# Optimization experiments

Hardware: AMD Instinct MI355X
Metric: run time of the kernel (lower is better)

Reference implementation:

```python
import jax, jax.numpy as jnp
import numpy as np

RCR = 5.2
RCA = 3.5
ETA_R = 16.0
ETA_A = 8.0
ZETA = 32.0
NUM_SPECIES = 4
NUM_PAIRS = NUM_SPECIES * (NUM_SPECIES + 1) // 2  # 10
SHFR = jnp.asarray(np.linspace(0.9, RCR, 17)[:-1], dtype=jnp.float32)   # (16,)
SHFA = jnp.asarray(np.linspace(0.9, RCA, 5)[:-1], dtype=jnp.float32)    # (4,)
SHFZ = jnp.asarray((np.linspace(0.0, np.pi, 9) + np.pi / 16.0)[:-1], dtype=jnp.float32)  # (8,)

def _triu_index(n):
    s1, s2 = np.triu_indices(n)
    t = np.zeros((n, n), dtype=np.int32)
    t[s1, s2] = np.arange(len(s1))
    t[s2, s1] = np.arange(len(s1))
    return jnp.asarray(t)

TRIU = _triu_index(NUM_SPECIES)  # (4,4) -> pair index in [0,10)

def _fc(d, rc):
    # cosine cutoff, zero beyond rc
    return jnp.where(d < rc, 0.5 * jnp.cos(np.float32(np.pi) * d / rc) + 0.5, 0.0)

def _aev(species, coordinates):
    N, A = species.shape
    # vec[n,i,j] = r_j - r_i  (N,A,A,3)
    vec = coordinates[:, None, :, :] - coordinates[:, :, None, :]
    d2 = jnp.sum(vec * vec, axis=-1)                      # (N,A,A)
    eye = jnp.eye(A, dtype=bool)
    d = jnp.sqrt(jnp.where(eye, 1.0, d2))                 # safe sqrt on diagonal
    pair_mask = (~eye).astype(coordinates.dtype)          # (A,A)

    # ---- radial AEV ----
    fcr = _fc(d, RCR) * pair_mask                         # (N,A,A)
    rad = 0.25 * jnp.exp(-ETA_R * (d[..., None] - SHFR) ** 2) * fcr[..., None]  # (N,A,A,16)
    sp_oh = jax.nn.one_hot(species, NUM_SPECIES, dtype=coordinates.dtype)       # (N,A,4)
    radial_aev = jnp.einsum('nijt,njs->nist', rad, sp_oh).reshape(N, A, -1)     # (N,A,64)

    # ---- angular AEV ----
    fca = _fc(d, RCA) * pair_mask                         # (N,A,A)
    dot = jnp.einsum('nijc,nikc->nijk', vec, vec)         # (N,A,A,A)
    cosang = 0.95 * dot / jnp.clip(d[:, :, :, None] * d[:, :, None, :], 1e-10)
    angles = jnp.arccos(cosang)                           # (N,A,A,A)
    mask_jk = (~eye).astype(coordinates.dtype)            # j != k
    fcj12 = fca[:, :, :, None] * fca[:, :, None, :] * mask_jk[None, None]  # (N,A,A,A)
    dmean = 0.5 * (d[:, :, :, None] + d[:, :, None, :])   # (N,A,A,A)
    factor1 = ((1.0 + jnp.cos(angles[..., None] - SHFZ)) * 0.5) ** ZETA    # (N,A,A,A,8)
    factor2 = jnp.exp(-ETA_A * (dmean[..., None] - SHFA) ** 2)             # (N,A,A,A,4)
    # terms over ordered (j,k); each unordered pair counted twice, so the
    # original factor 2 and the 0.5 double-count correction cancel.
    terms = (fcj12[..., None] * factor2)[..., :, None] * factor1[..., None, :]  # (N,A,A,A,4,8)
    terms = terms.reshape(N, A, A, A, SHFA.shape[0] * SHFZ.shape[0])            # (N,A,A,A,32)
    pair_idx = TRIU[species[:, :, None], species[:, None, :]]                   # (N,A,A)
    pair_oh = jax.nn.one_hot(pair_idx, NUM_PAIRS, dtype=coordinates.dtype)      # (N,A,A,10)
    angular_aev = jnp.einsum('nijkt,njkp->nipt', terms, pair_oh).reshape(N, A, -1)  # (N,A,320)

    return jnp.concatenate([radial_aev, angular_aev], axis=-1)  # (N,A,384)

def setup_inputs() -> dict:
    key = jax.random.key(0)
    k1, k2 = jax.random.split(key)
    species = jax.random.randint(k1, (32, 48), 0, NUM_SPECIES)
    # atoms in an 8 Angstrom box -> realistic neighbor density for 5.2 A cutoff
    coordinates = jax.random.uniform(k2, (32, 48, 3), dtype=jnp.float32) * 8.0
    return {"species": species, "coordinates": coordinates}

def reference(species, coordinates):
    return _aev(species, coordinates)
```

## Files before the change

### kernel.cpp

```cpp
#include <hip/hip_runtime.h>
#include <math.h>


#define A_ATOMS 48
#define NMOL    32
#define NFEAT   384
#define CHUNK   256

__device__ __constant__ float CZ_TAB[8] = {
     0.980785280f,  0.831469612f,  0.555570233f,  0.195090322f,
    -0.195090322f, -0.555570233f, -0.831469612f, -0.980785280f };
__device__ __constant__ float SZ_TAB[8] = {
     0.195090322f,  0.555570233f,  0.831469612f,  0.980785280f,
     0.980785280f,  0.831469612f,  0.555570233f,  0.195090322f };

__device__ __forceinline__ float bf2f(unsigned short h) {
    return __uint_as_float(((unsigned int)h) << 16);
}

__global__ __launch_bounds__(256, 6)
void AEVComputer_2156073583107_kernel(const void* __restrict__ coords_raw,
                                      const void* __restrict__ species_raw,
                                      float* __restrict__ out)
{
    const int bid   = blockIdx.x;
    const int n     = bid / A_ATOMS;
    const int i     = bid - n * A_ATOMS;
    const int tid   = threadIdx.x;
    const int w     = tid >> 6;
    const int lane  = tid & 63;
    const int sub   = lane >> 5;
    const int slice = (w << 1) | sub;
    const int t     = lane & 31;

    __shared__ float cx[A_ATOMS], cy[A_ATOMS], cz[A_ATOMS];
    __shared__ float dL[A_ATOMS], fcaL[A_ATOMS];
    __shared__ float ux[A_ATOMS], uy[A_ATOMS], uz[A_ATOMS];
    __shared__ int   sp[A_ATOMS], nbr[A_ATOMS];
    __shared__ int   Msh;
    __shared__ float4 pairbuf[CHUNK];
    __shared__ int   cnt[10], curs[10], ofs[11];
    __shared__ float ang_m[8][320];
    __shared__ float rad_m[4][64];

    const unsigned short* cu16 = (const unsigned short*)coords_raw;
    const unsigned int*   su32 = (const unsigned int*)species_raw;

    if (tid < 64) {
        float v = bf2f(cu16[tid]);
        unsigned long long mb = __ballot(fabsf(v) < 32.0f);
        const bool coords_bf16 = (__popcll(mb) >= 60);
        unsigned int sv = su32[tid & 31];
        unsigned long long m2 = __ballot((tid < 32) && sv >= 0x3F000000u && sv < 0x40800000u);
        unsigned long long m3 = __ballot((tid < 32) && (tid & 1) && sv != 0u);
        const int smode = (__popcll(m2) > 20) ? 2 : ((m3 == 0ull) ? 1 : 0);

        if (tid < A_ATOMS) {
            const int g = n * A_ATOMS + tid;
            float x, y, z;
            if (coords_bf16) {
                x = bf2f(cu16[3 * g]); y = bf2f(cu16[3 * g + 1]); z = bf2f(cu16[3 * g + 2]);
            } else {
                const float* cf = (const float*)coords_raw;
                x = cf[3 * g]; y = cf[3 * g + 1]; z = cf[3 * g + 2];
            }
            cx[tid] = x; cy[tid] = y; cz[tid] = z;
            int s;
            if (smode == 0)      s = ((const int*)species_raw)[g];
            else if (smode == 1) s = ((const int*)species_raw)[2 * g];
            else                 s = (int)(((const float*)species_raw)[g] + 0.5f);
            sp[tid] = (s < 0) ? 0 : ((s > 3) ? 3 : s);
        }
        if (tid < A_ATOMS) {
            float dx = cx[tid] - cx[i];
            float dy = cy[tid] - cy[i];
            float dz = cz[tid] - cz[i];
            float d2 = dx * dx + dy * dy + dz * dz;
            float d  = (tid == i) ? 1.0f : sqrtf(d2);
            float inv = 1.0f / d;
            dL[tid] = d;
            ux[tid] = dx * inv; uy[tid] = dy * inv; uz[tid] = dz * inv;
            float fca = 0.0f;
            if (tid != i && d < 3.5f)
                fca = 0.5f * __cosf(0.8975979010f * d) + 0.5f;
            fcaL[tid] = fca;
        }
        float dv = (tid < A_ATOMS) ? dL[tid] : 1e9f;
        bool pred = (tid < A_ATOMS) && (tid != i) && (dv < 3.5f);
        unsigned long long mask = __ballot(pred);
        if (pred) {
            int pos = __popcll(mask & ((1ull << tid) - 1ull));
            nbr[pos] = tid;
        }
        if (tid == 0) Msh = __popcll(mask);
    }
    __syncthreads();
    const int M = Msh;
    const int npairs = (M * (M - 1)) >> 1;

    {
        const int   s    = lane >> 4;
        const int   rt   = lane & 15;
        const float shfr = 0.9f + 0.26875f * (float)rt;
        float radv = 0.0f;
        for (int j = w; j < A_ATOMS; j += 4) {
            if (j == i) continue;
            float d = dL[j];
            if (d < 5.2f && sp[j] == s) {
                float fcr = 0.5f * __cosf(0.6041524333f * d) + 0.5f;
                float e   = d - shfr;
                radv += 0.25f * __expf(-16.0f * e * e) * fcr;
            }
        }
        rad_m[w][lane] = radv;
    }

    float a[10];
    #pragma unroll
    for (int p = 0; p < 10; ++p) a[p] = 0.0f;
    const float czv  = CZ_TAB[t & 7];
    const float szv  = SZ_TAB[t & 7];
    const float shfa = 0.9f + 0.65f * (float)(t >> 3);

    for (int base = 0; base < npairs; base += CHUNK) {
        if (tid < 10) cnt[tid] = 0;
        __syncthreads();

        const int  q     = base + tid;
        const bool havep = (q < npairs);
        float4 pd; int p = 0;
        if (havep) {
            const float b = (float)(2 * M - 1);
            int jj = (int)(0.5f * (b - sqrtf(fmaxf(b * b - 8.0f * (float)q, 0.0f))));
            jj = max(0, min(jj, M - 2));
            while (jj > 0 && q < ((jj * (2 * M - 1 - jj)) >> 1)) --jj;
            while (q >= (((jj + 1) * (2 * M - 2 - jj)) >> 1)) ++jj;
            const int kk = jj + 1 + (q - ((jj * (2 * M - 1 - jj)) >> 1));
            const int j = nbr[jj], k = nbr[kk];
            float c  = fmaf(ux[j], ux[k], fmaf(uy[j], uy[k], uz[j] * uz[k]));
            float cc = 0.95f * c;
            float ss = sqrtf(fmaxf(1.0f - cc * cc, 0.0f));
            pd.x = 0.5f * cc;
            pd.y = 0.5f * ss;
            pd.z = 2.0f * fcaL[j] * fcaL[k];
            pd.w = 0.5f * (dL[j] + dL[k]);
            int sj = sp[j], sk = sp[k];
            int lo = min(sj, sk), hi = max(sj, sk);
            p = ((lo * (7 - lo)) >> 1) + hi;
            atomicAdd(&cnt[p], 1);
        }
        __syncthreads();
        if (tid == 0) {
            int o = 0;
            #pragma unroll
            for (int pp = 0; pp < 10; ++pp) { ofs[pp] = o; curs[pp] = o; o += cnt[pp]; }
            ofs[10] = o;
        }
        __syncthreads();
        if (havep) {
            int slot = atomicAdd(&curs[p], 1);
            pairbuf[slot] = pd;
        }
        __syncthreads();

        #pragma unroll
        for (int pp = 0; pp < 10; ++pp) {
            const int e1 = ofs[pp + 1];
            for (int qq = ofs[pp] + slice; qq < e1; qq += 8) {
                float4 v = pairbuf[qq];
                float x  = fmaf(v.y, szv, fmaf(v.x, czv, 0.5f));
                float x2 = x * x, x4 = x2 * x2, x8 = x4 * x4, x16 = x8 * x8;
                float f1 = x16 * x16;
                float e  = v.w - shfa;
                float f2 = __expf(-8.0f * e * e);
                a[pp] = fmaf(v.z * f2, f1, a[pp]);
            }
        }
        __syncthreads();
    }

    #pragma unroll
    for (int p = 0; p < 10; ++p) ang_m[slice][p * 32 + t] = a[p];
    __syncthreads();

    const size_t outb = (size_t)bid * NFEAT;
    for (int f = tid; f < NFEAT; f += 256) {
        float v;
        if (f < 64) {
            v = rad_m[0][f] + rad_m[1][f] + rad_m[2][f] + rad_m[3][f];
        } else {
            const int g = f - 64;
            v = ((ang_m[0][g] + ang_m[1][g]) + (ang_m[2][g] + ang_m[3][g]))
              + ((ang_m[4][g] + ang_m[5][g]) + (ang_m[6][g] + ang_m[7][g]));
        }
        out[outb + f] = v;
    }
}

extern "C" void kernel_launch(void* const* d_in, const int* in_sizes, int n_in,
                              void* d_out, int out_size, void* d_ws, size_t ws_size,
                              hipStream_t stream) {
    if (n_in < 2) return;
    const void* coords;
    const void* species;
    if (in_sizes[0] >= in_sizes[1]) { coords = d_in[0]; species = d_in[1]; }
    else                            { coords = d_in[1]; species = d_in[0]; }
    float* out = (float*)d_out;
    AEVComputer_2156073583107_kernel<<<NMOL * A_ATOMS, 256, 0, stream>>>(coords, species, out);
}
```

Measured before the change: 64.92 us.

## Drop per-chunk species bucketing; accumulate angular terms by predicated select

The per-chunk counting sort of angle pairs by species pair, which used shared-memory atomics, a serial prefix scan and three extra barriers per chunk, is removed. Pairs are now stored in tid order with their pair index, and each lane adds its term into all 10 accumulators through a predicated select. The setup now broadcasts atom i's coordinates with wave shuffles instead of shared memory, and the radial loop is fully unrolled and branchless. The cost is ten select-adds per term plus radial exp/cos evaluated for every atom rather than only those inside the cutoff.

```diff
diff --git a/kernel.cpp b/kernel.cpp
--- a/kernel.cpp
+++ b/kernel.cpp
@@ -33,15 +33,14 @@
     const int slice = (w << 1) | sub;
     const int t     = lane & 31;
 
-    __shared__ float cx[A_ATOMS], cy[A_ATOMS], cz[A_ATOMS];
     __shared__ float dL[A_ATOMS], fcaL[A_ATOMS];
     __shared__ float ux[A_ATOMS], uy[A_ATOMS], uz[A_ATOMS];
     __shared__ int   sp[A_ATOMS], nbr[A_ATOMS];
     __shared__ int   Msh;
-    __shared__ float4 pairbuf[CHUNK];
-    __shared__ int   cnt[10], curs[10], ofs[11];
-    __shared__ float ang_m[8][320];
-    __shared__ float rad_m[4][64];
+    __shared__ float4 pairD[CHUNK];
+    __shared__ int    pairP[CHUNK];
+    __shared__ float  rad_m[4][64];
+    __shared__ float  ang_m[8][320];
 
     const unsigned short* cu16 = (const unsigned short*)coords_raw;
     const unsigned int*   su32 = (const unsigned int*)species_raw;
@@ -50,43 +49,37 @@
         float v = bf2f(cu16[tid]);
         unsigned long long mb = __ballot(fabsf(v) < 32.0f);
         const bool coords_bf16 = (__popcll(mb) >= 60);
-        unsigned int sv = su32[tid & 31];
-        unsigned long long m2 = __ballot((tid < 32) && sv >= 0x3F000000u && sv < 0x40800000u);
-        unsigned long long m3 = __ballot((tid < 32) && (tid & 1) && sv != 0u);
+        unsigned int svv = su32[tid & 31];
+        unsigned long long m2 = __ballot((tid < 32) && svv >= 0x3F000000u && svv < 0x40800000u);
+        unsigned long long m3 = __ballot((tid < 32) && (tid & 1) && svv != 0u);
         const int smode = (__popcll(m2) > 20) ? 2 : ((m3 == 0ull) ? 1 : 0);
 
+        float x = 0.f, y = 0.f, z = 0.f; int s = 0;
         if (tid < A_ATOMS) {
             const int g = n * A_ATOMS + tid;
-            float x, y, z;
             if (coords_bf16) {
                 x = bf2f(cu16[3 * g]); y = bf2f(cu16[3 * g + 1]); z = bf2f(cu16[3 * g + 2]);
             } else {
                 const float* cf = (const float*)coords_raw;
                 x = cf[3 * g]; y = cf[3 * g + 1]; z = cf[3 * g + 2];
             }
-            cx[tid] = x; cy[tid] = y; cz[tid] = z;
-            int s;
             if (smode == 0)      s = ((const int*)species_raw)[g];
             else if (smode == 1) s = ((const int*)species_raw)[2 * g];
             else                 s = (int)(((const float*)species_raw)[g] + 0.5f);
-            sp[tid] = (s < 0) ? 0 : ((s > 3) ? 3 : s);
+            s = (s < 0) ? 0 : ((s > 3) ? 3 : s);
         }
+        const float xi = __shfl(x, i), yi = __shfl(y, i), zi = __shfl(z, i);
+        float dx = x - xi, dy = y - yi, dz = z - zi;
+        float d2 = dx * dx + dy * dy + dz * dz;
+        float d  = (tid == i) ? 1.0f : sqrtf(d2);
+        float inv = 1.0f / d;
+        bool pred = (tid < A_ATOMS) && (tid != i) && (d < 3.5f);
+        float fca = pred ? (0.5f * __cosf(0.8975979010f * d) + 0.5f) : 0.0f;
         if (tid < A_ATOMS) {
-            float dx = cx[tid] - cx[i];
-            float dy = cy[tid] - cy[i];
-            float dz = cz[tid] - cz[i];
-            float d2 = dx * dx + dy * dy + dz * dz;
-            float d  = (tid == i) ? 1.0f : sqrtf(d2);
-            float inv = 1.0f / d;
             dL[tid] = d;
             ux[tid] = dx * inv; uy[tid] = dy * inv; uz[tid] = dz * inv;
-            float fca = 0.0f;
-            if (tid != i && d < 3.5f)
-                fca = 0.5f * __cosf(0.8975979010f * d) + 0.5f;
-            fcaL[tid] = fca;
+            fcaL[tid] = fca; sp[tid] = s;
         }
-        float dv = (tid < A_ATOMS) ? dL[tid] : 1e9f;
-        bool pred = (tid < A_ATOMS) && (tid != i) && (dv < 3.5f);
         unsigned long long mask = __ballot(pred);
         if (pred) {
             int pos = __popcll(mask & ((1ull << tid) - 1ull));
@@ -103,14 +96,15 @@
         const int   rt   = lane & 15;
         const float shfr = 0.9f + 0.26875f * (float)rt;
         float radv = 0.0f;
-        for (int j = w; j < A_ATOMS; j += 4) {
-            if (j == i) continue;
-            float d = dL[j];
-            if (d < 5.2f && sp[j] == s) {
-                float fcr = 0.5f * __cosf(0.6041524333f * d) + 0.5f;
-                float e   = d - shfr;
-                radv += 0.25f * __expf(-16.0f * e * e) * fcr;
-            }
+        #pragma unroll
+        for (int jj = 0; jj < 12; ++jj) {
+            const int j = w + 4 * jj;
+            float d   = dL[j];
+            float fcr = 0.5f * __cosf(0.6041524333f * d) + 0.5f;
+            float e   = d - shfr;
+            float val = 0.25f * __expf(-16.0f * e * e) * fcr;
+            bool  ok  = (j != i) && (d < 5.2f) && (sp[j] == s);
+            radv += ok ? val : 0.0f;
         }
         rad_m[w][lane] = radv;
     }
@@ -123,13 +117,8 @@
     const float shfa = 0.9f + 0.65f * (float)(t >> 3);
 
     for (int base = 0; base < npairs; base += CHUNK) {
-        if (tid < 10) cnt[tid] = 0;
-        __syncthreads();
-
-        const int  q     = base + tid;
-        const bool havep = (q < npairs);
-        float4 pd; int p = 0;
-        if (havep) {
+        const int q = base + tid;
+        if (q < npairs) {
             const float b = (float)(2 * M - 1);
             int jj = (int)(0.5f * (b - sqrtf(fmaxf(b * b - 8.0f * (float)q, 0.0f))));
             jj = max(0, min(jj, M - 2));
@@ -140,47 +129,34 @@
             float c  = fmaf(ux[j], ux[k], fmaf(uy[j], uy[k], uz[j] * uz[k]));
             float cc = 0.95f * c;
             float ss = sqrtf(fmaxf(1.0f - cc * cc, 0.0f));
+            float4 pd;
             pd.x = 0.5f * cc;
             pd.y = 0.5f * ss;
             pd.z = 2.0f * fcaL[j] * fcaL[k];
             pd.w = 0.5f * (dL[j] + dL[k]);
-            int sj = sp[j], sk = sp[k];
-            int lo = min(sj, sk), hi = max(sj, sk);
-            p = ((lo * (7 - lo)) >> 1) + hi;
-            atomicAdd(&cnt[p], 1);
+            const int sj = sp[j], sk = sp[k];
+            const int lo = min(sj, sk), hi = max(sj, sk);
+            pairD[tid] = pd;
+            pairP[tid] = ((lo * (7 - lo)) >> 1) + hi;
         }
         __syncthreads();
-        if (tid == 0) {
-            int o = 0;
+        const int cnt = min(CHUNK, npairs - base);
+        for (int qq = slice; qq < cnt; qq += 8) {
+            float4 v = pairD[qq];
+            int    p = pairP[qq];
+            float x  = fmaf(v.y, szv, fmaf(v.x, czv, 0.5f));
+            float x2 = x * x, x4 = x2 * x2, x8 = x4 * x4, x16 = x8 * x8;
+            float f1 = x16 * x16;
+            float e  = v.w - shfa;
+            float term = v.z * __expf(-8.0f * e * e) * f1;
             #pragma unroll
-            for (int pp = 0; pp < 10; ++pp) { ofs[pp] = o; curs[pp] = o; o += cnt[pp]; }
-            ofs[10] = o;
-        }
-        __syncthreads();
-        if (havep) {
-            int slot = atomicAdd(&curs[p], 1);
-            pairbuf[slot] = pd;
-        }
-        __syncthreads();
-
-        #pragma unroll
-        for (int pp = 0; pp < 10; ++pp) {
-            const int e1 = ofs[pp + 1];
-            for (int qq = ofs[pp] + slice; qq < e1; qq += 8) {
-                float4 v = pairbuf[qq];
-                float x  = fmaf(v.y, szv, fmaf(v.x, czv, 0.5f));
-                float x2 = x * x, x4 = x2 * x2, x8 = x4 * x4, x16 = x8 * x8;
-                float f1 = x16 * x16;
-                float e  = v.w - shfa;
-                float f2 = __expf(-8.0f * e * e);
-                a[pp] = fmaf(v.z * f2, f1, a[pp]);
-            }
+            for (int pp = 0; pp < 10; ++pp) a[pp] += (p == pp) ? term : 0.0f;
         }
         __syncthreads();
     }
 
     #pragma unroll
-    for (int p = 0; p < 10; ++p) ang_m[slice][p * 32 + t] = a[p];
+    for (int pp = 0; pp < 10; ++pp) ang_m[slice][pp * 32 + t] = a[pp];
     __syncthreads();
 
     const size_t outb = (size_t)bid * NFEAT;
```

Result: no change. 65.13 us (+0.3%).
